# Kernel tuning notes

Hardware: AMD Instinct MI355X
Metric: run time of the kernel (lower is better)

The kernel has to match this reference:

```python
import jax, jax.numpy as jnp
import numpy as np

B, T, C, H, W = 2, 2048, 2048, 16, 512
D = C // H  # head_dim = 128

def setup_inputs() -> dict:
    key = jax.random.key(0)
    k1, k2, k3 = jax.random.split(key, 3)
    x = jax.random.normal(k1, (B, T, C), dtype=jnp.float32)
    w_attn = jax.random.normal(k2, (C, 3 * C), dtype=jnp.float32) * 0.02
    w_proj = jax.random.normal(k3, (C, C), dtype=jnp.float32) * 0.02
    # standard RoPE tables: [T, D] with halves repeated
    inv_freq = 1.0 / (10000.0 ** (jnp.arange(0, D, 2, dtype=jnp.float32) / D))
    freqs = jnp.outer(jnp.arange(T, dtype=jnp.float32), inv_freq)  # [T, D/2]
    emb = jnp.concatenate([freqs, freqs], axis=-1)  # [T, D]
    return {"x": x, "freqs_cos": jnp.cos(emb), "freqs_sin": jnp.sin(emb),
            "w_attn": w_attn, "w_proj": w_proj}

def _rotate_half(t):
    return jnp.concatenate([-t[..., D // 2:], t[..., :D // 2]], axis=-1)

def reference(x, freqs_cos, freqs_sin, w_attn, w_proj):
    qkv = x @ w_attn  # [B,T,3C]
    q, k, v = jnp.split(qkv, 3, axis=-1)
    # [B,T,C] -> [B,H,T,D]
    q = q.reshape(B, T, H, D).transpose(0, 2, 1, 3)
    k = k.reshape(B, T, H, D).transpose(0, 2, 1, 3)
    v = v.reshape(B, T, H, D).transpose(0, 2, 1, 3)
    cos = freqs_cos[None, None, :, :]  # [1,1,T,D]
    sin = freqs_sin[None, None, :, :]
    q = q * cos + _rotate_half(q) * sin
    k = k * cos + _rotate_half(k) * sin
    scores = jnp.einsum('bhqd,bhkd->bhqk', q, k) / jnp.sqrt(jnp.float32(D))
    i = jnp.arange(T)[:, None]
    j = jnp.arange(T)[None, :]
    band = (j <= i) & (j > i - W)  # causal sliding window of width W
    scores = jnp.where(band[None, None, :, :], scores, -jnp.inf)
    att = jax.nn.softmax(scores, axis=-1)
    y = jnp.einsum('bhqk,bhkd->bhqd', att, v)
    y = y.transpose(0, 2, 1, 3).reshape(B, T, C)
    return y @ w_proj
```

## Files before the change

kernel.cpp:

```cpp
#include <hip/hip_runtime.h>
#include <stdint.h>

#define B_ 2
#define T_ 2048
#define C_ 2048
#define H_ 16
#define D_ 128
#define W_ 512
#define M_ (B_*T_)
#define N1_ (3*C_)

typedef short bf16x8 __attribute__((ext_vector_type(8)));
typedef unsigned short u16x8 __attribute__((ext_vector_type(8)));
typedef float f32x4 __attribute__((ext_vector_type(4)));

#define SB() __builtin_amdgcn_sched_barrier(0)

__device__ __forceinline__ unsigned short f2bf(float f) {
  union { float f; unsigned u; } v; v.f = f;
  unsigned r = v.u + 0x7fffu + ((v.u >> 16) & 1u);
  return (unsigned short)(r >> 16);
}
__device__ __forceinline__ float bf2f(unsigned short b) {
  union { unsigned u; float f; } v; v.u = ((unsigned)b) << 16;
  return v.f;
}

__device__ __forceinline__ void gload_lds16(const void* g, void* l) {
  __builtin_amdgcn_global_load_lds((const __attribute__((address_space(1))) void*)g,
                                   (__attribute__((address_space(3))) void*)l, 16, 0, 0);
}

__global__ void k_cvt(const float* __restrict__ s, unsigned short* __restrict__ d, int n) {
  int i = (blockIdx.x * blockDim.x + threadIdx.x) * 8;
  if (i >= n) return;
  float4 a = *(const float4*)(s + i);
  float4 b = *(const float4*)(s + i + 4);
  u16x8 o;
  o[0]=f2bf(a.x); o[1]=f2bf(a.y); o[2]=f2bf(a.z); o[3]=f2bf(a.w);
  o[4]=f2bf(b.x); o[5]=f2bf(b.y); o[6]=f2bf(b.z); o[7]=f2bf(b.w);
  *(u16x8*)(d + i) = o;
}

__global__ void k_tcvt(const float* __restrict__ s, unsigned short* __restrict__ d, int R, int Cc) {
  __shared__ float tile[32][33];
  int c0 = blockIdx.x * 32, r0 = blockIdx.y * 32;
  int tx = threadIdx.x & 31, ty = threadIdx.x >> 5;
  #pragma unroll
  for (int j = 0; j < 32; j += 8) tile[ty + j][tx] = s[(size_t)(r0 + ty + j) * Cc + c0 + tx];
  __syncthreads();
  #pragma unroll
  for (int j = 0; j < 32; j += 8) d[(size_t)(c0 + ty + j) * R + r0 + tx] = f2bf(tile[tx][ty + j]);
}

template<int ROWS, int K>
__device__ __forceinline__ void stage_half(const unsigned short* __restrict__ gbase,
                                           int row0, int kt, int kh,
                                           unsigned short* region, int tid, int sw) {
  const char* gsrc = (const char*)(gbase + (size_t)row0 * K + kt * 64 + kh * 32);
  {
    int o = tid * 16, s = o ^ sw;
    gload_lds16(gsrc + (size_t)(s >> 6) * (K * 2) + (s & 63), (char*)region + o);
  }
  if (ROWS == 256) {
    int o = (512 + tid) * 16, s = o ^ sw;
    gload_lds16(gsrc + (size_t)(s >> 6) * (K * 2) + (s & 63), (char*)region + o);
  }
}

template<bool F32OUT, int K, int Ntot>
__global__ __launch_bounds__(512, 2) void k_gemm8(const unsigned short* __restrict__ A,
                                                  const unsigned short* __restrict__ Bt,
                                                  void* __restrict__ Cp) {
  __shared__ unsigned short As[2][2][256 * 32];
  __shared__ unsigned short Bs[2][2][256 * 32];
  const int tid = threadIdx.x, lane = tid & 63, wv = tid >> 6;
  const int wm = wv >> 2, wn = wv & 3;
  const int lr = lane & 15, lg = lane >> 4;
  const int sw = tid & 32;
  const int fofs = lr * 64 + ((lg * 16) ^ ((lr & 8) << 2));
  const int aoff = wm * 128 * 64 + fofs;
  const int boff = wn * 64 * 64 + fofs;

  const int nwg = gridDim.x;
  const int nbx = Ntot >> 8;
  const int q = nwg >> 3, r = nwg & 7;
  const int xcd = blockIdx.x & 7, off = blockIdx.x >> 3;
  const int bid = (xcd < r ? xcd * (q + 1) : r * (q + 1) + (xcd - r) * q) + off;
  const int bm0 = (bid / nbx) << 8;
  const int bn0 = (bid % nbx) << 8;

  f32x4 acc[8][4];
  #pragma unroll
  for (int i = 0; i < 8; ++i)
    #pragma unroll
    for (int j = 0; j < 4; ++j)
      #pragma unroll
      for (int e = 0; e < 4; ++e) acc[i][j][e] = 0.f;

  constexpr int NT = K >> 6;

  stage_half<256, K>(A,  bm0, 0, 0, As[0][0], tid, sw);
  stage_half<256, K>(Bt, bn0, 0, 0, Bs[0][0], tid, sw);
  stage_half<256, K>(Bt, bn0, 0, 1, Bs[0][1], tid, sw);
  stage_half<256, K>(A,  bm0, 0, 1, As[0][1], tid, sw);
  stage_half<256, K>(Bt, bn0, 1, 0, Bs[1][0], tid, sw);
  stage_half<256, K>(A,  bm0, 1, 0, As[1][0], tid, sw);
  stage_half<256, K>(Bt, bn0, 1, 1, Bs[1][1], tid, sw);
  asm volatile("s_waitcnt vmcnt(4)" ::: "memory");
  __builtin_amdgcn_s_barrier();

  bf16x8 Xa[4], Xb[4], Ya[4];
  #pragma unroll
  for (int j = 0; j < 4; ++j) Xb[j] = *(const bf16x8*)((const char*)Bs[0][0] + boff + j * 1024);
  #pragma unroll
  for (int i = 0; i < 4; ++i) Xa[i] = *(const bf16x8*)((const char*)As[0][0] + aoff + i * 1024);

  #pragma unroll 2
  for (int t = 0; t < NT; ++t) {
    const int p = t & 1;
    asm volatile("s_waitcnt lgkmcnt(0)" ::: "memory");
    SB();
    __builtin_amdgcn_s_setprio(1);
    #pragma unroll
    for (int i = 0; i < 4; ++i)
      #pragma unroll
      for (int j = 0; j < 4; ++j)
        acc[i][j] = __builtin_amdgcn_mfma_f32_16x16x32_bf16(Xa[i], Xb[j], acc[i][j], 0, 0, 0);
    __builtin_amdgcn_s_setprio(0);
    #pragma unroll
    for (int i = 0; i < 4; ++i) Ya[i] = *(const bf16x8*)((const char*)As[p][0] + aoff + (i + 4) * 1024);
    if (t + 1 < NT) stage_half<256, K>(A, bm0, t + 1, 1, As[p ^ 1][1], tid, sw);
    __builtin_amdgcn_s_barrier();

    asm volatile("s_waitcnt lgkmcnt(0)" ::: "memory");
    SB();
    __builtin_amdgcn_s_setprio(1);
    #pragma unroll
    for (int i = 0; i < 4; ++i)
      #pragma unroll
      for (int j = 0; j < 4; ++j)
        acc[i + 4][j] = __builtin_amdgcn_mfma_f32_16x16x32_bf16(Ya[i], Xb[j], acc[i + 4][j], 0, 0, 0);
    __builtin_amdgcn_s_setprio(0);
    #pragma unroll
    for (int j = 0; j < 4; ++j) Xb[j] = *(const bf16x8*)((const char*)Bs[p][1] + boff + j * 1024);
    #pragma unroll
    for (int i = 0; i < 4; ++i) Xa[i] = *(const bf16x8*)((const char*)As[p][1] + aoff + i * 1024);
    if (t + 2 < NT) stage_half<256, K>(Bt, bn0, t + 2, 0, Bs[p][0], tid, sw);
    __builtin_amdgcn_s_barrier();

    asm volatile("s_waitcnt lgkmcnt(0)" ::: "memory");
    SB();
    __builtin_amdgcn_s_setprio(1);
    #pragma unroll
    for (int i = 0; i < 4; ++i)
      #pragma unroll
      for (int j = 0; j < 4; ++j)
        acc[i][j] = __builtin_amdgcn_mfma_f32_16x16x32_bf16(Xa[i], Xb[j], acc[i][j], 0, 0, 0);
    __builtin_amdgcn_s_setprio(0);
    #pragma unroll
    for (int i = 0; i < 4; ++i) Ya[i] = *(const bf16x8*)((const char*)As[p][1] + aoff + (i + 4) * 1024);
    if (t + 2 < NT) stage_half<256, K>(A, bm0, t + 2, 0, As[p][0], tid, sw);
    __builtin_amdgcn_s_barrier();

    asm volatile("s_waitcnt lgkmcnt(0)" ::: "memory");
    SB();
    __builtin_amdgcn_s_setprio(1);
    #pragma unroll
    for (int i = 0; i < 4; ++i)
      #pragma unroll
      for (int j = 0; j < 4; ++j)
        acc[i + 4][j] = __builtin_amdgcn_mfma_f32_16x16x32_bf16(Ya[i], Xb[j], acc[i + 4][j], 0, 0, 0);
    __builtin_amdgcn_s_setprio(0);
    if (t < NT - 2) asm volatile("s_waitcnt vmcnt(4)" ::: "memory");
    else            asm volatile("s_waitcnt vmcnt(0)" ::: "memory");
    #pragma unroll
    for (int j = 0; j < 4; ++j) Xb[j] = *(const bf16x8*)((const char*)Bs[p ^ 1][0] + boff + j * 1024);
    #pragma unroll
    for (int i = 0; i < 4; ++i) Xa[i] = *(const bf16x8*)((const char*)As[p ^ 1][0] + aoff + i * 1024);
    if (t + 2 < NT) stage_half<256, K>(Bt, bn0, t + 2, 1, Bs[p][1], tid, sw);
    __builtin_amdgcn_s_barrier();
  }
  asm volatile("s_waitcnt lgkmcnt(0)" ::: "memory");

  #pragma unroll
  for (int i = 0; i < 8; ++i)
    #pragma unroll
    for (int j = 0; j < 4; ++j) {
      int m = bm0 + wm * 128 + i * 16 + lg * 4;
      int n = bn0 + wn * 64 + j * 16 + lr;
      #pragma unroll
      for (int e = 0; e < 4; ++e) {
        if (F32OUT) ((float*)Cp)[(size_t)(m + e) * Ntot + n] = acc[i][j][e];
        else ((unsigned short*)Cp)[(size_t)(m + e) * Ntot + n] = f2bf(acc[i][j][e]);
      }
    }
}

template<int K, int Ntot>
__global__ __launch_bounds__(512, 4) void k_gemmS(const unsigned short* __restrict__ A,
                                                  const unsigned short* __restrict__ Bt,
                                                  float* __restrict__ Cp) {
  __shared__ unsigned short As[2][2][128 * 32];
  __shared__ unsigned short Bs[2][2][128 * 32];
  const int tid = threadIdx.x, lane = tid & 63, wv = tid >> 6;
  const int wm = wv >> 1, wn = wv & 1;
  const int lr = lane & 15, lg = lane >> 4;
  const int sw = tid & 32;
  const int fofs = lr * 64 + ((lg * 16) ^ ((lr & 8) << 2));
  const int aoff = wm * 32 * 64 + fofs;
  const int boff = wn * 64 * 64 + fofs;

  const int nwg = gridDim.x;
  const int nbx = Ntot >> 7;
  const int q = nwg >> 3, r = nwg & 7;
  const int xcd = blockIdx.x & 7, off = blockIdx.x >> 3;
  const int bid = (xcd < r ? xcd * (q + 1) : r * (q + 1) + (xcd - r) * q) + off;
  const int bm0 = (bid / nbx) << 7;
  const int bn0 = (bid % nbx) << 7;

  f32x4 acc[2][4];
  #pragma unroll
  for (int i = 0; i < 2; ++i)
    #pragma unroll
    for (int j = 0; j < 4; ++j)
      #pragma unroll
      for (int e = 0; e < 4; ++e) acc[i][j][e] = 0.f;

  constexpr int NT = K >> 6;

  auto stage_tile = [&](int kt, int rr) {
    stage_half<128, K>(A,  bm0, kt, 0, As[rr][0], tid, sw);
    stage_half<128, K>(Bt, bn0, kt, 0, Bs[rr][0], tid, sw);
    stage_half<128, K>(A,  bm0, kt, 1, As[rr][1], tid, sw);
    stage_half<128, K>(Bt, bn0, kt, 1, Bs[rr][1], tid, sw);
  };

  stage_tile(0, 0);
  asm volatile("s_waitcnt vmcnt(0)" ::: "memory");
  __builtin_amdgcn_s_barrier();

  for (int t = 0; t < NT; ++t) {
    const int p = t & 1;
    if (t + 1 < NT) stage_tile(t + 1, p ^ 1);

    bf16x8 af[2], bfr[4];
    #pragma unroll
    for (int kh = 0; kh < 2; ++kh) {
      #pragma unroll
      for (int i = 0; i < 2; ++i) af[i] = *(const bf16x8*)((const char*)As[p][kh] + aoff + i * 1024);
      #pragma unroll
      for (int j = 0; j < 4; ++j) bfr[j] = *(const bf16x8*)((const char*)Bs[p][kh] + boff + j * 1024);
      asm volatile("s_waitcnt lgkmcnt(0)" ::: "memory");
      SB();
      __builtin_amdgcn_s_setprio(1);
      #pragma unroll
      for (int i = 0; i < 2; ++i)
        #pragma unroll
        for (int j = 0; j < 4; ++j)
          acc[i][j] = __builtin_amdgcn_mfma_f32_16x16x32_bf16(af[i], bfr[j], acc[i][j], 0, 0, 0);
      __builtin_amdgcn_s_setprio(0);
    }
    asm volatile("s_waitcnt vmcnt(0)" ::: "memory");
    __builtin_amdgcn_s_barrier();
  }

  #pragma unroll
  for (int i = 0; i < 2; ++i)
    #pragma unroll
    for (int j = 0; j < 4; ++j) {
      int m = bm0 + wm * 32 + i * 16 + lg * 4;
      int n = bn0 + wn * 64 + j * 16 + lr;
      #pragma unroll
      for (int e = 0; e < 4; ++e)
        Cp[(size_t)(m + e) * Ntot + n] = acc[i][j][e];
    }
}

__global__ __launch_bounds__(256) void k_reorg(const unsigned short* __restrict__ qkv,
                        const float* __restrict__ fcos, const float* __restrict__ fsin,
                        unsigned short* __restrict__ q_r, unsigned short* __restrict__ k_r,
                        unsigned short* __restrict__ v_t) {
  const int bh = blockIdx.x, b = bh >> 4, h = bh & 15;
  const int t0 = blockIdx.y * 64;
  const int tid = threadIdx.x;
  __shared__ unsigned short vt[64][136];
  #pragma unroll
  for (int p = 0; p < 4; ++p) {
    int idx = p * 256 + tid;
    int tl = idx >> 4, sg = idx & 15;
    int t = t0 + tl, d0 = sg * 8;
    float sgn = (d0 < 64) ? -1.f : 1.f;
    float4 c0v = *(const float4*)(fcos + t * D_ + d0);
    float4 c1v = *(const float4*)(fcos + t * D_ + d0 + 4);
    float4 s0v = *(const float4*)(fsin + t * D_ + d0);
    float4 s1v = *(const float4*)(fsin + t * D_ + d0 + 4);
    float cs[8] = {c0v.x,c0v.y,c0v.z,c0v.w,c1v.x,c1v.y,c1v.z,c1v.w};
    float sn[8] = {s0v.x,s0v.y,s0v.z,s0v.w,s1v.x,s1v.y,s1v.z,s1v.w};
    #pragma unroll
    for (int w = 0; w < 2; ++w) {
      const unsigned short* src = qkv + (size_t)(b*T_ + t) * N1_ + w*C_ + h*D_;
      u16x8 a  = *(const u16x8*)(src + d0);
      u16x8 pr = *(const u16x8*)(src + (d0 ^ 64));
      u16x8 o;
      #pragma unroll
      for (int e = 0; e < 8; ++e)
        o[e] = f2bf(bf2f(a[e]) * cs[e] + sgn * bf2f(pr[e]) * sn[e]);
      unsigned short* dst = (w ? k_r : q_r) + (size_t)((b*H_ + h)*T_ + t) * D_ + d0;
      *(u16x8*)dst = o;
    }
    const unsigned short* vsrc = qkv + (size_t)(b*T_ + t) * N1_ + 2*C_ + h*D_ + d0;
    *(u16x8*)&vt[tl][d0] = *(const u16x8*)vsrc;
  }
  __syncthreads();
  #pragma unroll
  for (int p = 0; p < 4; ++p) {
    int idx = p * 256 + tid;
    int sg = idx & 7, d = idx >> 3;
    u16x8 o;
    #pragma unroll
    for (int e = 0; e < 8; ++e) o[e] = vt[sg*8 + e][d];
    *(u16x8*)(v_t + (size_t)((b*H_ + h)*D_ + d) * T_ + t0 + sg*8) = o;
  }
}

__global__ __launch_bounds__(512) void k_attn(const unsigned short* __restrict__ q_r,
                       const unsigned short* __restrict__ k_r,
                       const unsigned short* __restrict__ v_t,
                       unsigned short* __restrict__ y) {
  const int bh = blockIdx.x, b = bh >> 4, h = bh & 15;
  const int q0 = blockIdx.y * 128;
  const int tid = threadIdx.x, lane = tid & 63, wv = tid >> 6;
  const int lr = lane & 15, lg = lane >> 4;

  __shared__ unsigned short Ks[2][64 * 128];
  __shared__ unsigned short Vs[128 * 64];
  __shared__ unsigned short Ps[8 * 16 * 64];

  const size_t bhT = (size_t)(b*H_ + h) * T_;
  const size_t bhD = (size_t)(b*H_ + h) * D_;
  const unsigned short* qbase = q_r + (bhT + q0 + wv*16 + lr) * D_;
  bf16x8 qf[4];
  #pragma unroll
  for (int kk = 0; kk < 4; ++kk) qf[kk] = *(const bf16x8*)(qbase + kk*32 + lg*8);

  f32x4 o[8];
  #pragma unroll
  for (int i = 0; i < 8; ++i)
    #pragma unroll
    for (int e = 0; e < 4; ++e) o[i][e] = 0.f;
  float m_run[4], l_sum[4];
  #pragma unroll
  for (int e = 0; e < 4; ++e) { m_run[e] = -1e30f; l_sum[e] = 0.f; }

  const int i_min = q0 + wv*16, i_max = i_min + 15;
  int kt_lo = q0 - (W_ - 1); if (kt_lo < 0) kt_lo = 0; kt_lo &= ~63;
  const float scale = 0.08838834764831845f;

  unsigned short* Ps_w = Ps + wv * 1024;

  auto stage_k = [&](int kt, int buf) {
    #pragma unroll
    for (int c = 0; c < 2; ++c) {
      int ob = (c * 512 + tid) * 16;
      int row = ob >> 8, slot = (ob >> 4) & 15;
      int cb = slot ^ ((row & 7) << 1);
      gload_lds16(k_r + (bhT + kt + row) * D_ + cb * 8, (char*)Ks[buf] + ob);
    }
  };
  auto stage_v = [&](int kt) {
    #pragma unroll
    for (int c = 0; c < 2; ++c) {
      int ob = (c * 512 + tid) * 16;
      int d = ob >> 7, slot = (ob >> 4) & 7;
      int cb = slot ^ (d & 7);
      gload_lds16(v_t + (bhD + d) * T_ + kt + cb * 8, (char*)Vs + ob);
    }
  };

  stage_k(kt_lo, 0);
  int cur = 0;
  for (int kt = kt_lo; kt < q0 + 128; kt += 64) {
    const bool has_next = (kt + 64 < q0 + 128);
    stage_v(kt);
    if (has_next) stage_k(kt + 64, cur ^ 1);
    if (has_next) asm volatile("s_waitcnt vmcnt(4)" ::: "memory");
    else          asm volatile("s_waitcnt vmcnt(2)" ::: "memory");
    __builtin_amdgcn_s_barrier();

    const bool live = (kt <= i_max) && (kt + 63 >= i_min - (W_ - 1));
    float sv[4][4];
    if (live) {
      const unsigned short* Kc = Ks[cur];
      f32x4 s[4];
      #pragma unroll
      for (int ct = 0; ct < 4; ++ct)
        #pragma unroll
        for (int e = 0; e < 4; ++e) s[ct][e] = 0.f;
      #pragma unroll
      for (int kk = 0; kk < 4; ++kk) {
        #pragma unroll
        for (int ct = 0; ct < 4; ++ct) {
          bf16x8 kf = *(const bf16x8*)&Kc[(ct*16 + lr)*128 + ((kk*4 + lg) ^ ((lr & 7) << 1))*8];
          s[ct] = __builtin_amdgcn_mfma_f32_16x16x32_bf16(qf[kk], kf, s[ct], 0, 0, 0);
        }
      }
      float mnew[4];
      int grow = 0;
      #pragma unroll
      for (int e = 0; e < 4; ++e) {
        int i = i_min + lg*4 + e;
        float rm = -1e30f;
        #pragma unroll
        for (int ct = 0; ct < 4; ++ct) {
          int j = kt + ct*16 + lr;
          bool ok = (j <= i) && (j > i - W_);
          sv[e][ct] = ok ? s[ct][e] * scale : -1e30f;
          rm = fmaxf(rm, sv[e][ct]);
        }
        #pragma unroll
        for (int msk = 1; msk < 16; msk <<= 1) rm = fmaxf(rm, __shfl_xor(rm, msk));
        mnew[e] = fmaxf(m_run[e], rm);
        grow |= (mnew[e] > m_run[e]) ? 1 : 0;
      }
      if (__any(grow)) {
        #pragma unroll
        for (int e = 0; e < 4; ++e) {
          float fac = __expf(m_run[e] - mnew[e]);
          l_sum[e] *= fac;
          m_run[e] = mnew[e];
          #pragma unroll
          for (int nt = 0; nt < 8; ++nt) o[nt][e] *= fac;
        }
      }
      #pragma unroll
      for (int e = 0; e < 4; ++e) {
        int prow = lg*4 + e;
        float rs = 0.f;
        #pragma unroll
        for (int ct = 0; ct < 4; ++ct) {
          float pv = (sv[e][ct] > -1e29f) ? __expf(sv[e][ct] - m_run[e]) : 0.f;
          rs += pv;
          Ps_w[prow*64 + ((ct*2 + (lr >> 3)) ^ (prow & 7))*8 + (lr & 7)] = f2bf(pv);
        }
        #pragma unroll
        for (int msk = 1; msk < 16; msk <<= 1) rs += __shfl_xor(rs, msk);
        l_sum[e] += rs;
      }
    }
    if (has_next) asm volatile("s_waitcnt vmcnt(2)" ::: "memory");
    else          asm volatile("s_waitcnt vmcnt(0)" ::: "memory");
    __builtin_amdgcn_s_barrier();

    if (live) {
      asm volatile("s_waitcnt lgkmcnt(0)" ::: "memory"); SB();
      #pragma unroll
      for (int kk = 0; kk < 2; ++kk) {
        bf16x8 pf = *(const bf16x8*)&Ps_w[lr*64 + ((kk*4 + lg) ^ (lr & 7))*8];
        #pragma unroll
        for (int nt = 0; nt < 8; ++nt) {
          bf16x8 vf = *(const bf16x8*)&Vs[(nt*16 + lr)*64 + ((kk*4 + lg) ^ (lr & 7))*8];
          o[nt] = __builtin_amdgcn_mfma_f32_16x16x32_bf16(pf, vf, o[nt], 0, 0, 0);
        }
      }
    }
    asm volatile("s_waitcnt lgkmcnt(0)" ::: "memory");
    __builtin_amdgcn_s_barrier();
    cur ^= 1;
  }

  #pragma unroll
  for (int nt = 0; nt < 8; ++nt) {
    #pragma unroll
    for (int e = 0; e < 4; ++e) {
      int t = q0 + wv*16 + lg*4 + e;
      int d = nt*16 + lr;
      y[(size_t)(b*T_ + t) * C_ + h*D_ + d] = f2bf(o[nt][e] / l_sum[e]);
    }
  }
}

extern "C" void kernel_launch(void* const* d_in, const int* in_sizes, int n_in,
                              void* d_out, int out_size, void* d_ws, size_t ws_size,
                              hipStream_t stream) {
  const float* x      = (const float*)d_in[0];
  const float* fcos   = (const float*)d_in[1];
  const float* fsin   = (const float*)d_in[2];
  const float* w_attn = (const float*)d_in[3];
  const float* w_proj = (const float*)d_in[4];
  float* out = (float*)d_out;

  char* ws = (char*)d_ws;
  unsigned short* x_bf = (unsigned short*)(ws);
  unsigned short* wa_t = (unsigned short*)(ws + 16777216ull);
  unsigned short* wp_t = (unsigned short*)(ws + 41943040ull);
  unsigned short* qkv  = (unsigned short*)(ws + 50331648ull);
  unsigned short* q_r  = (unsigned short*)(ws + 100663296ull);
  unsigned short* k_r  = (unsigned short*)(ws + 117440512ull);
  unsigned short* v_t  = (unsigned short*)(ws + 134217728ull);
  unsigned short* y_bf = x_bf;

  k_cvt<<<dim3(4096), dim3(256), 0, stream>>>(x, x_bf, M_*C_);
  k_tcvt<<<dim3(192, 64), dim3(256), 0, stream>>>(w_attn, wa_t, C_, N1_);
  k_tcvt<<<dim3(64, 64), dim3(256), 0, stream>>>(w_proj, wp_t, C_, C_);
  k_gemm8<false, C_, N1_><<<dim3(384), dim3(512), 0, stream>>>(x_bf, wa_t, qkv);
  k_reorg<<<dim3(32, 32), dim3(256), 0, stream>>>(qkv, fcos, fsin, q_r, k_r, v_t);
  k_attn<<<dim3(32, 16), dim3(512), 0, stream>>>(q_r, k_r, v_t, y_bf);
  k_gemmS<C_, C_><<<dim3(512), dim3(512), 0, stream>>>(y_bf, wp_t, out);
}
```

Before: 282.1 us.

## Fuse RoPE and head reshuffle into QKV GEMM epilogue; merge attention barriers

The QKV GEMM now remaps each wave's B-tile columns so a lane holds both halves of a rotary pair. RoPE is applied in the epilogue and Q/K are written straight into the per-head layout. V goes to a compact buffer and is transposed by a slimmer kernel, which removes the full qkv round trip and the RoPE work from the reorg pass. The attention loop also drops one barrier by waiting for V earlier and doing PV right after softmax. In exchange the epilogue does scattered 2-byte stores and cos/sin loads, and V loads are now exposed before QK.

Result: faster. 266.1 us (-5.7%).

```diff
diff --git a/kernel.cpp b/kernel.cpp
--- a/kernel.cpp
+++ b/kernel.cpp
@@ -68,10 +68,14 @@
   }
 }
 
-template<bool F32OUT, int K, int Ntot>
-__global__ __launch_bounds__(512, 2) void k_gemm8(const unsigned short* __restrict__ A,
+template<int K, int Ntot>
+__global__ __launch_bounds__(512, 2) void k_gemmF(const unsigned short* __restrict__ A,
                                                   const unsigned short* __restrict__ Bt,
-                                                  void* __restrict__ Cp) {
+                                                  const float* __restrict__ fcos,
+                                                  const float* __restrict__ fsin,
+                                                  unsigned short* __restrict__ q_r,
+                                                  unsigned short* __restrict__ k_r,
+                                                  unsigned short* __restrict__ vq) {
   __shared__ unsigned short As[2][2][256 * 32];
   __shared__ unsigned short Bs[2][2][256 * 32];
   const int tid = threadIdx.x, lane = tid & 63, wv = tid >> 6;
@@ -80,7 +84,10 @@
   const int sw = tid & 32;
   const int fofs = lr * 64 + ((lg * 16) ^ ((lr & 8) << 2));
   const int aoff = wm * 128 * 64 + fofs;
-  const int boff = wn * 64 * 64 + fofs;
+  int bofs[4];
+  #pragma unroll
+  for (int j = 0; j < 4; ++j)
+    bofs[j] = ((wn >> 1) * 128 + (wn & 1) * 32 + (j >> 1) * 64 + (j & 1) * 16) * 64 + fofs;
 
   const int nwg = gridDim.x;
   const int nbx = Ntot >> 8;
@@ -112,7 +119,7 @@
 
   bf16x8 Xa[4], Xb[4], Ya[4];
   #pragma unroll
-  for (int j = 0; j < 4; ++j) Xb[j] = *(const bf16x8*)((const char*)Bs[0][0] + boff + j * 1024);
+  for (int j = 0; j < 4; ++j) Xb[j] = *(const bf16x8*)((const char*)Bs[0][0] + bofs[j]);
   #pragma unroll
   for (int i = 0; i < 4; ++i) Xa[i] = *(const bf16x8*)((const char*)As[0][0] + aoff + i * 1024);
 
@@ -143,7 +150,7 @@
         acc[i + 4][j] = __builtin_amdgcn_mfma_f32_16x16x32_bf16(Ya[i], Xb[j], acc[i + 4][j], 0, 0, 0);
     __builtin_amdgcn_s_setprio(0);
     #pragma unroll
-    for (int j = 0; j < 4; ++j) Xb[j] = *(const bf16x8*)((const char*)Bs[p][1] + boff + j * 1024);
+    for (int j = 0; j < 4; ++j) Xb[j] = *(const bf16x8*)((const char*)Bs[p][1] + bofs[j]);
     #pragma unroll
     for (int i = 0; i < 4; ++i) Xa[i] = *(const bf16x8*)((const char*)As[p][1] + aoff + i * 1024);
     if (t + 2 < NT) stage_half<256, K>(Bt, bn0, t + 2, 0, Bs[p][0], tid, sw);
@@ -175,7 +182,7 @@
     if (t < NT - 2) asm volatile("s_waitcnt vmcnt(4)" ::: "memory");
     else            asm volatile("s_waitcnt vmcnt(0)" ::: "memory");
     #pragma unroll
-    for (int j = 0; j < 4; ++j) Xb[j] = *(const bf16x8*)((const char*)Bs[p ^ 1][0] + boff + j * 1024);
+    for (int j = 0; j < 4; ++j) Xb[j] = *(const bf16x8*)((const char*)Bs[p ^ 1][0] + bofs[j]);
     #pragma unroll
     for (int i = 0; i < 4; ++i) Xa[i] = *(const bf16x8*)((const char*)As[p ^ 1][0] + aoff + i * 1024);
     if (t + 2 < NT) stage_half<256, K>(Bt, bn0, t + 2, 1, Bs[p][1], tid, sw);
@@ -183,18 +190,43 @@
   }
   asm volatile("s_waitcnt lgkmcnt(0)" ::: "memory");
 
-  #pragma unroll
-  for (int i = 0; i < 8; ++i)
-    #pragma unroll
-    for (int j = 0; j < 4; ++j) {
-      int m = bm0 + wm * 128 + i * 16 + lg * 4;
-      int n = bn0 + wn * 64 + j * 16 + lr;
-      #pragma unroll
-      for (int e = 0; e < 4; ++e) {
-        if (F32OUT) ((float*)Cp)[(size_t)(m + e) * Ntot + n] = acc[i][j][e];
-        else ((unsigned short*)Cp)[(size_t)(m + e) * Ntot + n] = f2bf(acc[i][j][e]);
-      }
-    }
+  const int nb  = bn0 >> 11;
+  const int rem = bn0 & 2047;
+  const int b   = bm0 >> 11;
+  const int t0  = bm0 & 2047;
+  const int wcb = (wn >> 1) * 128 + (wn & 1) * 32;
+
+  if (nb == 2) {
+    #pragma unroll
+    for (int i = 0; i < 8; ++i)
+      #pragma unroll
+      for (int j = 0; j < 4; ++j) {
+        int col = rem + wcb + (j >> 1) * 64 + (j & 1) * 16 + lr;
+        #pragma unroll
+        for (int e = 0; e < 4; ++e) {
+          int t = t0 + wm * 128 + i * 16 + lg * 4 + e;
+          vq[((size_t)(b * T_ + t)) * C_ + col] = f2bf(acc[i][j][e]);
+        }
+      }
+  } else {
+    unsigned short* dst = nb ? k_r : q_r;
+    #pragma unroll
+    for (int i = 0; i < 8; ++i)
+      #pragma unroll
+      for (int j = 0; j < 4; ++j) {
+        int col = rem + wcb + (j >> 1) * 64 + (j & 1) * 16 + lr;
+        int head = col >> 7, d = col & 127;
+        float sgn = (j < 2) ? -1.f : 1.f;
+        #pragma unroll
+        for (int e = 0; e < 4; ++e) {
+          int t = t0 + wm * 128 + i * 16 + lg * 4 + e;
+          float c = fcos[t * D_ + d];
+          float s = fsin[t * D_ + d];
+          float out = acc[i][j][e] * c + sgn * acc[i][j ^ 2][e] * s;
+          dst[((size_t)(b * H_ + head) * T_ + t) * D_ + d] = f2bf(out);
+        }
+      }
+  }
 }
 
 template<int K, int Ntot>
@@ -277,10 +309,8 @@
     }
 }
 
-__global__ __launch_bounds__(256) void k_reorg(const unsigned short* __restrict__ qkv,
-                        const float* __restrict__ fcos, const float* __restrict__ fsin,
-                        unsigned short* __restrict__ q_r, unsigned short* __restrict__ k_r,
-                        unsigned short* __restrict__ v_t) {
+__global__ __launch_bounds__(256) void k_vt(const unsigned short* __restrict__ vq,
+                                            unsigned short* __restrict__ v_t) {
   const int bh = blockIdx.x, b = bh >> 4, h = bh & 15;
   const int t0 = blockIdx.y * 64;
   const int tid = threadIdx.x;
@@ -290,27 +320,7 @@
     int idx = p * 256 + tid;
     int tl = idx >> 4, sg = idx & 15;
     int t = t0 + tl, d0 = sg * 8;
-    float sgn = (d0 < 64) ? -1.f : 1.f;
-    float4 c0v = *(const float4*)(fcos + t * D_ + d0);
-    float4 c1v = *(const float4*)(fcos + t * D_ + d0 + 4);
-    float4 s0v = *(const float4*)(fsin + t * D_ + d0);
-    float4 s1v = *(const float4*)(fsin + t * D_ + d0 + 4);
-    float cs[8] = {c0v.x,c0v.y,c0v.z,c0v.w,c1v.x,c1v.y,c1v.z,c1v.w};
-    float sn[8] = {s0v.x,s0v.y,s0v.z,s0v.w,s1v.x,s1v.y,s1v.z,s1v.w};
-    #pragma unroll
-    for (int w = 0; w < 2; ++w) {
-      const unsigned short* src = qkv + (size_t)(b*T_ + t) * N1_ + w*C_ + h*D_;
-      u16x8 a  = *(const u16x8*)(src + d0);
-      u16x8 pr = *(const u16x8*)(src + (d0 ^ 64));
-      u16x8 o;
-      #pragma unroll
-      for (int e = 0; e < 8; ++e)
-        o[e] = f2bf(bf2f(a[e]) * cs[e] + sgn * bf2f(pr[e]) * sn[e]);
-      unsigned short* dst = (w ? k_r : q_r) + (size_t)((b*H_ + h)*T_ + t) * D_ + d0;
-      *(u16x8*)dst = o;
-    }
-    const unsigned short* vsrc = qkv + (size_t)(b*T_ + t) * N1_ + 2*C_ + h*D_ + d0;
-    *(u16x8*)&vt[tl][d0] = *(const u16x8*)vsrc;
+    *(u16x8*)&vt[tl][d0] = *(const u16x8*)(vq + (size_t)(b*T_ + t) * C_ + h*D_ + d0);
   }
   __syncthreads();
   #pragma unroll
@@ -384,8 +394,8 @@
     const bool has_next = (kt + 64 < q0 + 128);
     stage_v(kt);
     if (has_next) stage_k(kt + 64, cur ^ 1);
-    if (has_next) asm volatile("s_waitcnt vmcnt(4)" ::: "memory");
-    else          asm volatile("s_waitcnt vmcnt(2)" ::: "memory");
+    if (has_next) asm volatile("s_waitcnt vmcnt(2)" ::: "memory");
+    else          asm volatile("s_waitcnt vmcnt(0)" ::: "memory");
     __builtin_amdgcn_s_barrier();
 
     const bool live = (kt <= i_max) && (kt + 63 >= i_min - (W_ - 1));
@@ -447,12 +457,6 @@
         for (int msk = 1; msk < 16; msk <<= 1) rs += __shfl_xor(rs, msk);
         l_sum[e] += rs;
       }
-    }
-    if (has_next) asm volatile("s_waitcnt vmcnt(2)" ::: "memory");
-    else          asm volatile("s_waitcnt vmcnt(0)" ::: "memory");
-    __builtin_amdgcn_s_barrier();
-
-    if (live) {
       asm volatile("s_waitcnt lgkmcnt(0)" ::: "memory"); SB();
       #pragma unroll
       for (int kk = 0; kk < 2; ++kk) {
@@ -494,7 +498,7 @@
   unsigned short* x_bf = (unsigned short*)(ws);
   unsigned short* wa_t = (unsigned short*)(ws + 16777216ull);
   unsigned short* wp_t = (unsigned short*)(ws + 41943040ull);
-  unsigned short* qkv  = (unsigned short*)(ws + 50331648ull);
+  unsigned short* vq   = (unsigned short*)(ws + 50331648ull);
   unsigned short* q_r  = (unsigned short*)(ws + 100663296ull);
   unsigned short* k_r  = (unsigned short*)(ws + 117440512ull);
   unsigned short* v_t  = (unsigned short*)(ws + 134217728ull);
@@ -503,8 +507,8 @@
   k_cvt<<<dim3(4096), dim3(256), 0, stream>>>(x, x_bf, M_*C_);
   k_tcvt<<<dim3(192, 64), dim3(256), 0, stream>>>(w_attn, wa_t, C_, N1_);
   k_tcvt<<<dim3(64, 64), dim3(256), 0, stream>>>(w_proj, wp_t, C_, C_);
-  k_gemm8<false, C_, N1_><<<dim3(384), dim3(512), 0, stream>>>(x_bf, wa_t, qkv);
-  k_reorg<<<dim3(32, 32), dim3(256), 0, stream>>>(qkv, fcos, fsin, q_r, k_r, v_t);
+  k_gemmF<C_, N1_><<<dim3(384), dim3(512), 0, stream>>>(x_bf, wa_t, fcos, fsin, q_r, k_r, vq);
+  k_vt<<<dim3(32, 32), dim3(256), 0, stream>>>(vq, v_t);
   k_attn<<<dim3(32, 16), dim3(512), 0, stream>>>(q_r, k_r, v_t, y_bf);
   k_gemmS<C_, C_><<<dim3(512), dim3(512), 0, stream>>>(y_bf, wp_t, out);
 }
```
